# Performance work log

Measured on AMD Instinct MI355X. Metric: run time of the kernel, lower is better.

The kernel has to match this reference:

```python
import jax, jax.numpy as jnp
import numpy as np

# DeepSeek-V3-style gate config
TOP_K = 8
N_EXPERTS = 256
N_GROUP = 8
TOPK_GROUP = 4
ROUTED_SCALING = 2.5
EPS = 1e-20


def setup_inputs() -> dict:
    key = jax.random.key(0)
    k1, k2, k3 = jax.random.split(key, 3)
    S, H = 16384, 7168
    hidden_states = jax.random.normal(k1, (S, H), dtype=jnp.float32)
    weight = jax.random.normal(k2, (N_EXPERTS, H), dtype=jnp.float32) * 0.02
    e_score_correction_bias = jax.random.normal(k3, (N_EXPERTS,), dtype=jnp.float32) * 0.1
    return {"hidden_states": hidden_states, "weight": weight,
            "e_score_correction_bias": e_score_correction_bias}


def reference(hidden_states, weight, e_score_correction_bias):
    S = hidden_states.shape[0]
    group_size = N_EXPERTS // N_GROUP  # 32

    # gating GEMM: [S, E]
    router_logits = jnp.einsum('sh,eh->se', hidden_states, weight)
    # scoring_func == 'sigmoid'
    scores = jax.nn.sigmoid(router_logits)
    scores_for_choice = scores + e_score_correction_bias[None, :]

    # group scores: sum of top-2 biased scores within each group -> [S, G]
    grouped = scores_for_choice.reshape(S, N_GROUP, group_size)
    top2_vals, _ = jax.lax.top_k(grouped, 2)
    group_scores = top2_vals.sum(axis=-1)

    # select top `TOPK_GROUP` groups, build group mask
    _, group_idx = jax.lax.top_k(group_scores, TOPK_GROUP)  # [S, topk_group]
    group_mask = jnp.zeros((S, N_GROUP), dtype=scores.dtype)
    group_mask = group_mask.at[jnp.arange(S)[:, None], group_idx].set(1.0)
    score_mask = jnp.repeat(group_mask, group_size, axis=-1)  # [S, E]

    # masked top-k over experts; weights gathered from UNBIASED scores
    tmp_scores = jnp.where(score_mask > 0, scores_for_choice, 0.0)
    _, topk_idx = jax.lax.top_k(tmp_scores, TOP_K)  # [S, top_k]
    topk_weight = jnp.take_along_axis(scores, topk_idx, axis=1)

    # renormalize (top_k > 1 and norm_topk_prob) then scale (noaux_tc)
    denom = topk_weight.sum(axis=-1, keepdims=True) + EPS
    topk_weight = topk_weight / denom * ROUTED_SCALING
    return topk_weight, topk_idx
```

## Files before the change

### kernel.cpp

```cpp
#include <hip/hip_runtime.h>
#include <math.h>

#define H_DIM 7168
#define N_EXP 256
#define N_GRP 8
#define G_SZ  32
#define TOPK_G 4
#define TOPK   8
#define BM 64
#define BK 32
#define S_TOK 16384
#define NTILES (H_DIM / BK)
#define NSPLIT 4
#define NQ     (NTILES / NSPLIT)
#define ITILES 2
#define NINT   (NQ / ITILES)
#define TILE_W_BYTES 32768

#define SA_SCALE 256.0f
#define SW_SCALE 4096.0f
#define DESCALE  (1.0f / 1048576.0f)

__device__ __align__(256) char g_wimg[(size_t)NTILES * TILE_W_BYTES];
__device__ __align__(256) float g_part[NSPLIT * (size_t)S_TOK * N_EXP];

typedef __attribute__((ext_vector_type(8))) _Float16 f16x8;
typedef __attribute__((ext_vector_type(4))) float f32x4;
typedef __attribute__((ext_vector_type(4))) unsigned short u16x4;
typedef __attribute__((ext_vector_type(8))) unsigned short u16x8;

__device__ inline void split2h(float x, unsigned short& h, unsigned short& l) {
    _Float16 hf = (_Float16)x;
    _Float16 lf = (_Float16)(x - (float)hf);
    h = __builtin_bit_cast(unsigned short, hf);
    l = __builtin_bit_cast(unsigned short, lf);
}

__global__ __launch_bounds__(256)
void convert_w_kernel(const float* __restrict__ W) {
    int idx  = blockIdx.x * 256 + threadIdx.x;
    int e    = idx / (H_DIM / 8);
    int koct = idx - e * (H_DIM / 8);
    int k0   = koct * 8;
    int t    = k0 >> 5;
    int o    = (k0 >> 3) & 3;
    int lane = (e & 15) | (o << 4);
    int w    = e >> 5;
    int nj   = (e >> 4) & 1;
    const float* src = W + (size_t)e * H_DIM + k0;
    unsigned short h[8], l[8];
    #pragma unroll
    for (int j = 0; j < 8; ++j)
        split2h(src[j] * SW_SCALE, h[j], l[j]);
    char* base = g_wimg + (size_t)t * TILE_W_BYTES + (w << 12) + (lane << 4);
    *(u16x8*)(base + nj * 1024)       = u16x8{h[0],h[1],h[2],h[3],h[4],h[5],h[6],h[7]};
    *(u16x8*)(base + (2 + nj) * 1024) = u16x8{l[0],l[1],l[2],l[3],l[4],l[5],l[6],l[7]};
}

__global__ __launch_bounds__(512, 3)
void moe_gemm_quarter(const float* __restrict__ A)
{
    __shared__ __align__(128) char smem[2 * ITILES * 8192];

    const int tid   = threadIdx.x;
    const int lane  = tid & 63;
    const int wave  = tid >> 6;
    const int b     = blockIdx.x;
    const int kq    = b & 3;
    const int brow  = (b >> 2) * BM;

    const int fr   = lane & 15;
    const int fkb  = (lane >> 4) << 4;
    const int fswz = ((fr << 6) + fkb) ^ ((fr & 7) << 4);

    const int ar   = tid >> 3;
    const int akq  = tid & 7;
    const int aswz = ((ar << 6) + (akq << 3)) ^ ((ar & 7) << 4);
    const float4* Ag4 = reinterpret_cast<const float4*>(
        A + (size_t)(brow + ar) * H_DIM + kq * (H_DIM / NSPLIT)) + akq;

    const char* wsrc = g_wimg + (size_t)(kq * NQ) * TILE_W_BYTES
                       + (wave << 12) + (lane << 4);

    f32x4 acc[4][2] = {};

    auto writeA = [&](const float4& v, char* ab) {
        unsigned short h[4], l[4];
        split2h(v.x * SA_SCALE, h[0], l[0]); split2h(v.y * SA_SCALE, h[1], l[1]);
        split2h(v.z * SA_SCALE, h[2], l[2]); split2h(v.w * SA_SCALE, h[3], l[3]);
        *(u16x4*)(ab + aswz)        = u16x4{h[0], h[1], h[2], h[3]};
        *(u16x4*)(ab + 4096 + aswz) = u16x4{l[0], l[1], l[2], l[3]};
    };

    auto doTile = [&](int t, const char* ab) {
        const char* p = wsrc + (size_t)t * TILE_W_BYTES;
        f16x8 bh0 = *(const f16x8*)(p + 0);
        f16x8 bh1 = *(const f16x8*)(p + 1024);
        f16x8 bl0 = *(const f16x8*)(p + 2048);
        f16x8 bl1 = *(const f16x8*)(p + 3072);
        f16x8 ah[4];
        #pragma unroll
        for (int mi = 0; mi < 4; ++mi)
            ah[mi] = *(const f16x8*)(ab + mi * 1024 + fswz);
        __builtin_amdgcn_s_setprio(1);
        #pragma unroll
        for (int mi = 0; mi < 4; ++mi)
            acc[mi][0] = __builtin_amdgcn_mfma_f32_16x16x32_f16(ah[mi], bh0, acc[mi][0], 0, 0, 0);
        #pragma unroll
        for (int mi = 0; mi < 4; ++mi)
            acc[mi][1] = __builtin_amdgcn_mfma_f32_16x16x32_f16(ah[mi], bh1, acc[mi][1], 0, 0, 0);
        #pragma unroll
        for (int mi = 0; mi < 4; ++mi)
            acc[mi][0] = __builtin_amdgcn_mfma_f32_16x16x32_f16(ah[mi], bl0, acc[mi][0], 0, 0, 0);
        #pragma unroll
        for (int mi = 0; mi < 4; ++mi)
            acc[mi][1] = __builtin_amdgcn_mfma_f32_16x16x32_f16(ah[mi], bl1, acc[mi][1], 0, 0, 0);
        __builtin_amdgcn_s_setprio(0);
        f16x8 al[4];
        #pragma unroll
        for (int mi = 0; mi < 4; ++mi)
            al[mi] = *(const f16x8*)(ab + 4096 + mi * 1024 + fswz);
        __builtin_amdgcn_s_setprio(1);
        #pragma unroll
        for (int mi = 0; mi < 4; ++mi)
            acc[mi][0] = __builtin_amdgcn_mfma_f32_16x16x32_f16(al[mi], bh0, acc[mi][0], 0, 0, 0);
        #pragma unroll
        for (int mi = 0; mi < 4; ++mi)
            acc[mi][1] = __builtin_amdgcn_mfma_f32_16x16x32_f16(al[mi], bh1, acc[mi][1], 0, 0, 0);
        __builtin_amdgcn_s_setprio(0);
    };

    {
        float4 a0 = Ag4[0], a1 = Ag4[8];
        writeA(a0, smem);
        writeA(a1, smem + 8192);
        asm volatile("s_waitcnt lgkmcnt(0)" ::: "memory");
        __builtin_amdgcn_s_barrier();
    }

    #pragma unroll 1
    for (int i = 0; i < NINT; ++i) {
        char* cur = smem + (i & 1) * (ITILES * 8192);
        char* nxt = smem + ((i + 1) & 1) * (ITILES * 8192);
        const bool havenext = (i + 1 < NINT);
        const int ibase = (havenext ? i + 1 : i) * ITILES;

        doTile(i * ITILES, cur);
        {
            if (havenext) {
                float4 a0 = Ag4[(size_t)(ibase + 0) * 8];
                float4 a1 = Ag4[(size_t)(ibase + 1) * 8];
                writeA(a0, nxt);
                writeA(a1, nxt + 8192);
            }
        }
        doTile(i * ITILES + 1, cur + 8192);
        asm volatile("s_waitcnt lgkmcnt(0)" ::: "memory");
        __builtin_amdgcn_s_barrier();
    }

    float* pb = g_part + ((size_t)kq * S_TOK + brow) * N_EXP;
    #pragma unroll
    for (int mi = 0; mi < 4; ++mi)
        #pragma unroll
        for (int nj = 0; nj < 2; ++nj)
            #pragma unroll
            for (int q = 0; q < 4; ++q) {
                int row = mi * 16 + ((lane >> 4) << 2) + q;
                int col = (wave << 5) + (nj << 4) + (lane & 15);
                pb[row * N_EXP + col] = acc[mi][nj][q];
            }
}

__global__ __launch_bounds__(256)
void gate_kernel(const float* __restrict__ bias, float* __restrict__ out, int S)
{
    const int lane = threadIdx.x & 63;
    const int row  = (blockIdx.x * 256 + threadIdx.x) >> 6;

    const float4 p0 = *(const float4*)(g_part + (size_t)row * N_EXP + lane * 4);
    const float4 p1 = *(const float4*)(g_part + ((size_t)S_TOK + row) * N_EXP + lane * 4);
    const float4 p2 = *(const float4*)(g_part + (2 * (size_t)S_TOK + row) * N_EXP + lane * 4);
    const float4 p3 = *(const float4*)(g_part + (3 * (size_t)S_TOK + row) * N_EXP + lane * 4);
    const float4 b4 = *(const float4*)(bias + lane * 4);

    float s[4], v[4];
    float m1 = -1e30f, m2 = -1e30f;
    {
        const float* q0 = (const float*)&p0;
        const float* q1 = (const float*)&p1;
        const float* q2 = (const float*)&p2;
        const float* q3 = (const float*)&p3;
        const float* qb = (const float*)&b4;
        #pragma unroll
        for (int j = 0; j < 4; ++j) {
            float x = (((q0[j] + q1[j]) + q2[j]) + q3[j]) * DESCALE;
            s[j] = 1.0f / (1.0f + expf(-x));
            float sb = s[j] + qb[j];
            v[j] = sb;
            if (sb > m1) { m2 = m1; m1 = sb; } else if (sb > m2) { m2 = sb; }
        }
    }
    #pragma unroll
    for (int d = 1; d < 8; d <<= 1) {
        float om1 = __shfl_xor(m1, d), om2 = __shfl_xor(m2, d);
        float hi = fmaxf(m1, om1), lo = fminf(m1, om1);
        m1 = hi;
        m2 = fmaxf(lo, fmaxf(m2, om2));
    }
    float gs = m1 + m2;
    float gsv[8];
    #pragma unroll
    for (int g = 0; g < 8; ++g) gsv[g] = __shfl(gs, g << 3);

    unsigned gmask = 0;
    #pragma unroll
    for (int t = 0; t < TOPK_G; ++t) {
        float best = -1e30f; int bg = 0;
        #pragma unroll
        for (int g = 0; g < 8; ++g) {
            bool avail = !((gmask >> g) & 1);
            if (avail && gsv[g] > best) { best = gsv[g]; bg = g; }
        }
        gmask |= 1u << bg;
    }

    const bool sel = (gmask >> (lane >> 3)) & 1;
    #pragma unroll
    for (int j = 0; j < 4; ++j) v[j] = sel ? v[j] : 0.0f;

    float wv[TOPK]; int wi[TOPK]; float wsum = 0.0f;
    #pragma unroll
    for (int t = 0; t < TOPK; ++t) {
        float bv = v[0]; int bj = 0;
        #pragma unroll
        for (int j = 1; j < 4; ++j)
            if (v[j] > bv) { bv = v[j]; bj = j; }
        int bidx = (lane << 2) | bj;
        #pragma unroll
        for (int d = 32; d >= 1; d >>= 1) {
            float ov = __shfl_xor(bv, d);
            int   oi = __shfl_xor(bidx, d);
            if (ov > bv || (ov == bv && oi < bidx)) { bv = ov; bidx = oi; }
        }
        int ol = bidx >> 2, oj = bidx & 3;
        float sl = s[0];
        if (oj == 1) sl = s[1]; else if (oj == 2) sl = s[2]; else if (oj == 3) sl = s[3];
        float sv = __shfl(sl, ol);
        wv[t] = sv; wi[t] = bidx; wsum += sv;
        if (lane == ol) {
            if (oj == 0) v[0] = -1e30f; else if (oj == 1) v[1] = -1e30f;
            else if (oj == 2) v[2] = -1e30f; else v[3] = -1e30f;
        }
    }

    if (lane == 0) {
        float scale = 2.5f / (wsum + 1e-20f);
        #pragma unroll
        for (int t = 0; t < TOPK; ++t) {
            out[(size_t)row * TOPK + t] = wv[t] * scale;
            out[(size_t)S * TOPK + (size_t)row * TOPK + t] = (float)wi[t];
        }
    }
}

extern "C" void kernel_launch(void* const* d_in, const int* in_sizes, int n_in,
                              void* d_out, int out_size, void* d_ws, size_t ws_size,
                              hipStream_t stream) {
    const float* A    = (const float*)d_in[0];
    const float* W    = (const float*)d_in[1];
    const float* bias = (const float*)d_in[2];
    float* out = (float*)d_out;
    const int S = in_sizes[0] / H_DIM;

    convert_w_kernel<<<dim3(N_EXP * (H_DIM / 8) / 256), 256, 0, stream>>>(W);
    moe_gemm_quarter<<<dim3(NSPLIT * S / BM), 512, 0, stream>>>(A);
    gate_kernel<<<dim3(S / 4), 256, 0, stream>>>(bias, out, S);
}
```

Baseline: 222.8 us.

## Double GEMM row tile to 128 to reuse weight fragments across twice the rows

Raises the block row tile from 64 to 128 tokens, so each block loads the split weight fragments once and applies them to twice as many A rows. The accumulator array doubles and the A shared-memory tiles double, with launch bounds relaxed from 3 to 2 blocks per CU. The aim is to halve global weight-image traffic per token and amortise the per-tile weight loads, at the cost of more registers, lower occupancy, and half as many blocks in the grid.

New measurement: 208.7 us, median of 2. 6.3% less time.

```diff
diff --git a/kernel.cpp b/kernel.cpp
--- a/kernel.cpp
+++ b/kernel.cpp
@@ -7,7 +7,7 @@
 #define G_SZ  32
 #define TOPK_G 4
 #define TOPK   8
-#define BM 64
+#define BM 128
 #define BK 32
 #define S_TOK 16384
 #define NTILES (H_DIM / BK)
@@ -16,6 +16,7 @@
 #define ITILES 2
 #define NINT   (NQ / ITILES)
 #define TILE_W_BYTES 32768
+#define TILE_A_BYTES 16384
 
 #define SA_SCALE 256.0f
 #define SW_SCALE 4096.0f
@@ -57,10 +58,10 @@
     *(u16x8*)(base + (2 + nj) * 1024) = u16x8{l[0],l[1],l[2],l[3],l[4],l[5],l[6],l[7]};
 }
 
-__global__ __launch_bounds__(512, 3)
+__global__ __launch_bounds__(512, 2)
 void moe_gemm_quarter(const float* __restrict__ A)
 {
-    __shared__ __align__(128) char smem[2 * ITILES * 8192];
+    __shared__ __align__(128) char smem[2 * ITILES * TILE_A_BYTES];
 
     const int tid   = threadIdx.x;
     const int lane  = tid & 63;
@@ -78,19 +79,24 @@
     const int aswz = ((ar << 6) + (akq << 3)) ^ ((ar & 7) << 4);
     const float4* Ag4 = reinterpret_cast<const float4*>(
         A + (size_t)(brow + ar) * H_DIM + kq * (H_DIM / NSPLIT)) + akq;
+    const size_t ROW64 = (size_t)64 * (H_DIM / 4);
+
+    f32x4 acc[8][2] = {};
+
+    auto writeA2 = [&](const float4& v0, const float4& v1, char* ab) {
+        unsigned short h0[4], l0[4], h1[4], l1[4];
+        split2h(v0.x * SA_SCALE, h0[0], l0[0]); split2h(v0.y * SA_SCALE, h0[1], l0[1]);
+        split2h(v0.z * SA_SCALE, h0[2], l0[2]); split2h(v0.w * SA_SCALE, h0[3], l0[3]);
+        split2h(v1.x * SA_SCALE, h1[0], l1[0]); split2h(v1.y * SA_SCALE, h1[1], l1[1]);
+        split2h(v1.z * SA_SCALE, h1[2], l1[2]); split2h(v1.w * SA_SCALE, h1[3], l1[3]);
+        *(u16x4*)(ab + aswz)         = u16x4{h0[0], h0[1], h0[2], h0[3]};
+        *(u16x4*)(ab + 4096 + aswz)  = u16x4{h1[0], h1[1], h1[2], h1[3]};
+        *(u16x4*)(ab + 8192 + aswz)  = u16x4{l0[0], l0[1], l0[2], l0[3]};
+        *(u16x4*)(ab + 12288 + aswz) = u16x4{l1[0], l1[1], l1[2], l1[3]};
+    };
 
     const char* wsrc = g_wimg + (size_t)(kq * NQ) * TILE_W_BYTES
                        + (wave << 12) + (lane << 4);
-
-    f32x4 acc[4][2] = {};
-
-    auto writeA = [&](const float4& v, char* ab) {
-        unsigned short h[4], l[4];
-        split2h(v.x * SA_SCALE, h[0], l[0]); split2h(v.y * SA_SCALE, h[1], l[1]);
-        split2h(v.z * SA_SCALE, h[2], l[2]); split2h(v.w * SA_SCALE, h[3], l[3]);
-        *(u16x4*)(ab + aswz)        = u16x4{h[0], h[1], h[2], h[3]};
-        *(u16x4*)(ab + 4096 + aswz) = u16x4{l[0], l[1], l[2], l[3]};
-    };
 
     auto doTile = [&](int t, const char* ab) {
         const char* p = wsrc + (size_t)t * TILE_W_BYTES;
@@ -98,70 +104,74 @@
         f16x8 bh1 = *(const f16x8*)(p + 1024);
         f16x8 bl0 = *(const f16x8*)(p + 2048);
         f16x8 bl1 = *(const f16x8*)(p + 3072);
-        f16x8 ah[4];
-        #pragma unroll
-        for (int mi = 0; mi < 4; ++mi)
-            ah[mi] = *(const f16x8*)(ab + mi * 1024 + fswz);
-        __builtin_amdgcn_s_setprio(1);
-        #pragma unroll
-        for (int mi = 0; mi < 4; ++mi)
-            acc[mi][0] = __builtin_amdgcn_mfma_f32_16x16x32_f16(ah[mi], bh0, acc[mi][0], 0, 0, 0);
-        #pragma unroll
-        for (int mi = 0; mi < 4; ++mi)
-            acc[mi][1] = __builtin_amdgcn_mfma_f32_16x16x32_f16(ah[mi], bh1, acc[mi][1], 0, 0, 0);
-        #pragma unroll
-        for (int mi = 0; mi < 4; ++mi)
-            acc[mi][0] = __builtin_amdgcn_mfma_f32_16x16x32_f16(ah[mi], bl0, acc[mi][0], 0, 0, 0);
-        #pragma unroll
-        for (int mi = 0; mi < 4; ++mi)
-            acc[mi][1] = __builtin_amdgcn_mfma_f32_16x16x32_f16(ah[mi], bl1, acc[mi][1], 0, 0, 0);
-        __builtin_amdgcn_s_setprio(0);
-        f16x8 al[4];
-        #pragma unroll
-        for (int mi = 0; mi < 4; ++mi)
-            al[mi] = *(const f16x8*)(ab + 4096 + mi * 1024 + fswz);
-        __builtin_amdgcn_s_setprio(1);
-        #pragma unroll
-        for (int mi = 0; mi < 4; ++mi)
-            acc[mi][0] = __builtin_amdgcn_mfma_f32_16x16x32_f16(al[mi], bh0, acc[mi][0], 0, 0, 0);
-        #pragma unroll
-        for (int mi = 0; mi < 4; ++mi)
-            acc[mi][1] = __builtin_amdgcn_mfma_f32_16x16x32_f16(al[mi], bh1, acc[mi][1], 0, 0, 0);
-        __builtin_amdgcn_s_setprio(0);
+        #pragma unroll
+        for (int mb = 0; mb < 2; ++mb) {
+            f16x8 ah[4];
+            #pragma unroll
+            for (int m = 0; m < 4; ++m)
+                ah[m] = *(const f16x8*)(ab + (mb * 4 + m) * 1024 + fswz);
+            __builtin_amdgcn_s_setprio(1);
+            #pragma unroll
+            for (int m = 0; m < 4; ++m)
+                acc[mb*4+m][0] = __builtin_amdgcn_mfma_f32_16x16x32_f16(ah[m], bh0, acc[mb*4+m][0], 0, 0, 0);
+            #pragma unroll
+            for (int m = 0; m < 4; ++m)
+                acc[mb*4+m][1] = __builtin_amdgcn_mfma_f32_16x16x32_f16(ah[m], bh1, acc[mb*4+m][1], 0, 0, 0);
+            #pragma unroll
+            for (int m = 0; m < 4; ++m)
+                acc[mb*4+m][0] = __builtin_amdgcn_mfma_f32_16x16x32_f16(ah[m], bl0, acc[mb*4+m][0], 0, 0, 0);
+            #pragma unroll
+            for (int m = 0; m < 4; ++m)
+                acc[mb*4+m][1] = __builtin_amdgcn_mfma_f32_16x16x32_f16(ah[m], bl1, acc[mb*4+m][1], 0, 0, 0);
+            __builtin_amdgcn_s_setprio(0);
+            f16x8 al[4];
+            #pragma unroll
+            for (int m = 0; m < 4; ++m)
+                al[m] = *(const f16x8*)(ab + 8192 + (mb * 4 + m) * 1024 + fswz);
+            __builtin_amdgcn_s_setprio(1);
+            #pragma unroll
+            for (int m = 0; m < 4; ++m)
+                acc[mb*4+m][0] = __builtin_amdgcn_mfma_f32_16x16x32_f16(al[m], bh0, acc[mb*4+m][0], 0, 0, 0);
+            #pragma unroll
+            for (int m = 0; m < 4; ++m)
+                acc[mb*4+m][1] = __builtin_amdgcn_mfma_f32_16x16x32_f16(al[m], bh1, acc[mb*4+m][1], 0, 0, 0);
+            __builtin_amdgcn_s_setprio(0);
+        }
     };
 
     {
-        float4 a0 = Ag4[0], a1 = Ag4[8];
-        writeA(a0, smem);
-        writeA(a1, smem + 8192);
+        float4 a00 = Ag4[0],      a01 = Ag4[ROW64];
+        float4 a10 = Ag4[8],      a11 = Ag4[ROW64 + 8];
+        writeA2(a00, a01, smem);
+        writeA2(a10, a11, smem + TILE_A_BYTES);
         asm volatile("s_waitcnt lgkmcnt(0)" ::: "memory");
         __builtin_amdgcn_s_barrier();
     }
 
     #pragma unroll 1
     for (int i = 0; i < NINT; ++i) {
-        char* cur = smem + (i & 1) * (ITILES * 8192);
-        char* nxt = smem + ((i + 1) & 1) * (ITILES * 8192);
+        char* cur = smem + (i & 1) * (ITILES * TILE_A_BYTES);
+        char* nxt = smem + ((i + 1) & 1) * (ITILES * TILE_A_BYTES);
         const bool havenext = (i + 1 < NINT);
-        const int ibase = (havenext ? i + 1 : i) * ITILES;
+        const int ib = (havenext ? i + 1 : i) * ITILES;
 
         doTile(i * ITILES, cur);
-        {
-            if (havenext) {
-                float4 a0 = Ag4[(size_t)(ibase + 0) * 8];
-                float4 a1 = Ag4[(size_t)(ibase + 1) * 8];
-                writeA(a0, nxt);
-                writeA(a1, nxt + 8192);
-            }
-        }
-        doTile(i * ITILES + 1, cur + 8192);
+        if (havenext) {
+            float4 a00 = Ag4[(size_t)(ib + 0) * 8];
+            float4 a01 = Ag4[ROW64 + (size_t)(ib + 0) * 8];
+            float4 a10 = Ag4[(size_t)(ib + 1) * 8];
+            float4 a11 = Ag4[ROW64 + (size_t)(ib + 1) * 8];
+            writeA2(a00, a01, nxt);
+            writeA2(a10, a11, nxt + TILE_A_BYTES);
+        }
+        doTile(i * ITILES + 1, cur + TILE_A_BYTES);
         asm volatile("s_waitcnt lgkmcnt(0)" ::: "memory");
         __builtin_amdgcn_s_barrier();
     }
 
     float* pb = g_part + ((size_t)kq * S_TOK + brow) * N_EXP;
     #pragma unroll
-    for (int mi = 0; mi < 4; ++mi)
+    for (int mi = 0; mi < 8; ++mi)
         #pragma unroll
         for (int nj = 0; nj < 2; ++nj)
             #pragma unroll
```
